# Performance work log

Measured on AMD Instinct MI355X. Metric: run time of the kernel, lower is better.

## Reference

```python
import jax, jax.numpy as jnp
import numpy as np

THETA = 10000.0


def apply_rope(t):
    """Partial rotary on first head_dim//2 dims, interleaved pairs (rotary_embedding_torch).
    t: (B, H, S, D) float32."""
    B, H, S, D = t.shape
    rot_dim = D // 2  # RotaryEmbedding(head_dim // 2)
    inv_freq = 1.0 / (THETA ** (jnp.arange(0, rot_dim, 2, dtype=jnp.float32) / rot_dim))  # (rot_dim//2,)
    pos = jnp.arange(S, dtype=jnp.float32)
    freqs = pos[:, None] * inv_freq[None, :]            # (S, rot_dim//2)
    freqs = jnp.repeat(freqs, 2, axis=-1)               # (S, rot_dim) interleaved
    cos, sin = jnp.cos(freqs), jnp.sin(freqs)           # (S, rot_dim)
    t_rot, t_pass = t[..., :rot_dim], t[..., rot_dim:]
    x1 = t_rot[..., 0::2]
    x2 = t_rot[..., 1::2]
    rot_half = jnp.stack((-x2, x1), axis=-1).reshape(t_rot.shape)
    t_rot = t_rot * cos + rot_half * sin
    return jnp.concatenate([t_rot, t_pass], axis=-1)


def setup_inputs() -> dict:
    key = jax.random.key(0)
    k1, k2, k3, k4, k5 = jax.random.split(key, 5)
    B, S, Dm = 2, 2048, 1024
    scale = 1.0 / np.sqrt(Dm)
    return {
        "x": jax.random.normal(k1, (B, S, Dm), dtype=jnp.float32),
        "Wqkv": jax.random.normal(k2, (3 * Dm, Dm), dtype=jnp.float32) * scale,
        "bqkv": jax.random.normal(k3, (3 * Dm,), dtype=jnp.float32) * 0.01,
        "Wout": jax.random.normal(k4, (Dm, Dm), dtype=jnp.float32) * scale,
        "bout": jax.random.normal(k5, (Dm,), dtype=jnp.float32) * 0.01,
    }


def reference(x, Wqkv, bqkv, Wout, bout):
    B, S, Dm = x.shape
    H = 16
    Dh = Dm // H
    qkv = x @ Wqkv.T + bqkv                              # (B, S, 3*Dm)
    qkv = qkv.reshape(B, S, 3, H, Dh).transpose(2, 0, 3, 1, 4)  # (3, B, H, S, Dh)
    q, k, v = qkv[0], qkv[1], qkv[2]
    q = apply_rope(q.astype(jnp.float32))
    k = apply_rope(k.astype(jnp.float32))
    scores = jnp.einsum("bhqd,bhkd->bhqk", q, k) / jnp.sqrt(jnp.float32(Dh))
    attn = jax.nn.softmax(scores, axis=-1)
    out = jnp.einsum("bhqk,bhkd->bhqd", attn, v)         # (B, H, S, Dh)
    out = out.transpose(0, 2, 1, 3).reshape(B, S, Dm)
    return out @ Wout.T + bout
```

## Files before the change

kernel.cpp:

```cpp
#include <hip/hip_runtime.h>

#define S_LEN 2048
#define DMODEL 1024
#define NHEAD 16
#define DHEAD 64
#define BATCH 2
#define BH_TOT (BATCH * NHEAD)
#define TOK (BATCH * S_LEN)
#define NQKV (3 * DMODEL)

#define QSCALE 0.18033688011112042f

typedef float  f32x4  __attribute__((ext_vector_type(4)));
typedef __bf16 bf16x8 __attribute__((ext_vector_type(8)));
typedef __bf16 bf16x4 __attribute__((ext_vector_type(4)));
typedef __bf16 bf16x2 __attribute__((ext_vector_type(2)));
typedef short  s16x4  __attribute__((ext_vector_type(4)));

typedef __attribute__((address_space(1))) void* as1_ptr;
typedef __attribute__((address_space(3))) void* as3_ptr;

__device__ __forceinline__ void gl2lds16(const void* g, void* l) {
  __builtin_amdgcn_global_load_lds((as1_ptr)(void*)g, (as3_ptr)l, 16, 0, 0);
}

__device__ __forceinline__ f32x4 mfma32(bf16x8 a, bf16x8 b, f32x4 c) {
  return __builtin_amdgcn_mfma_f32_16x16x32_bf16(a, b, c, 0, 0, 0);
}
__device__ __forceinline__ f32x4 mfma16(bf16x4 a, bf16x4 b, f32x4 c) {
  return __builtin_amdgcn_mfma_f32_16x16x16bf16_1k(
      __builtin_bit_cast(s16x4, a), __builtin_bit_cast(s16x4, b), c, 0, 0, 0);
}

__global__ __launch_bounds__(256) void cvt_kernel(const float* __restrict__ src,
                                                  __bf16* __restrict__ dst, int n) {
  const int i = (blockIdx.x * 256 + threadIdx.x) * 4;
  if (i >= n) return;
  const f32x4 v = *(const f32x4*)(src + i);
  bf16x4 o;
  o[0] = (__bf16)v[0]; o[1] = (__bf16)v[1]; o[2] = (__bf16)v[2]; o[3] = (__bf16)v[3];
  *(bf16x4*)(dst + i) = o;
}

__device__ __forceinline__ void gemm_tile_128(const __bf16* __restrict__ A,
                                              const __bf16* __restrict__ Bw,
                                              const int Kd, const int tileM, const int tileN,
                                              __bf16* As, __bf16* Bs, f32x4 acc[4][4]) {
  const int t    = threadIdx.x;
  const int lane = t & 63;
  const int wave = t >> 6;
  const int quad = lane >> 4;
  const int c    = lane & 15;
  const int wm   = (wave >> 1) << 6;
  const int wn   = (wave & 1) << 6;

  const int u0 = t, u1 = t + 256;
  const __bf16* gA0 = A  + (size_t)(tileM + (u0 >> 2)) * Kd + (u0 & 3) * 8;
  const __bf16* gA1 = A  + (size_t)(tileM + (u1 >> 2)) * Kd + (u1 & 3) * 8;
  const __bf16* gB0 = Bw + (size_t)(tileN + (u0 >> 2)) * Kd + (u0 & 3) * 8;
  const __bf16* gB1 = Bw + (size_t)(tileN + (u1 >> 2)) * Kd + (u1 & 3) * 8;
  __bf16* lA0 = As + u0 * 8; __bf16* lA1 = As + u1 * 8;
  __bf16* lB0 = Bs + u0 * 8; __bf16* lB1 = Bs + u1 * 8;

  for (int k0 = 0; k0 < Kd; k0 += 32) {
    gl2lds16(gA0 + k0, lA0);
    gl2lds16(gA1 + k0, lA1);
    gl2lds16(gB0 + k0, lB0);
    gl2lds16(gB1 + k0, lB1);
    __syncthreads();
    bf16x8 af[4], bfr[4];
#pragma unroll
    for (int mt = 0; mt < 4; ++mt)
      af[mt] = *(const bf16x8*)(As + (wm + mt * 16 + c) * 32 + quad * 8);
#pragma unroll
    for (int nt = 0; nt < 4; ++nt)
      bfr[nt] = *(const bf16x8*)(Bs + (wn + nt * 16 + c) * 32 + quad * 8);
#pragma unroll
    for (int mt = 0; mt < 4; ++mt)
#pragma unroll
      for (int nt = 0; nt < 4; ++nt)
        acc[mt][nt] = mfma32(af[mt], bfr[nt], acc[mt][nt]);
    __syncthreads();
  }
}

__global__ __launch_bounds__(256) void gemm_qkv_kernel(const __bf16* __restrict__ xb,
                                                       const __bf16* __restrict__ Wb,
                                                       const float* __restrict__ bias,
                                                       __bf16* __restrict__ Qb,
                                                       __bf16* __restrict__ Kb,
                                                       __bf16* __restrict__ Vtb) {
  __shared__ __align__(16) __bf16 As[128 * 32];
  __shared__ __align__(16) __bf16 Bs[128 * 32];
  f32x4 acc[4][4];
#pragma unroll
  for (int i = 0; i < 4; ++i)
#pragma unroll
    for (int j = 0; j < 4; ++j) acc[i][j] = (f32x4){0.f, 0.f, 0.f, 0.f};

  const int tileM = blockIdx.y * 128;
  const int tileN = blockIdx.x * 128;
  gemm_tile_128(xb, Wb, DMODEL, tileM, tileN, As, Bs, acc);

  const int t = threadIdx.x;
  const int lane = t & 63, wave = t >> 6;
  const int quad = lane >> 4, c = lane & 15;
  const int wm = (wave >> 1) << 6, wn = (wave & 1) << 6;

#pragma unroll
  for (int nt = 0; nt < 4; ++nt) {
    const int col = tileN + wn + nt * 16 + c;
    const float bv = bias[col];
    const int which = col >> 10;
    const int h  = (col >> 6) & 15;
    const int dh = col & 63;
    if (which == 2) {
#pragma unroll
      for (int mt = 0; mt < 4; ++mt) {
        const int row0 = tileM + wm + mt * 16 + quad * 4;
        const int bb = row0 >> 11;
        const int ss = row0 & (S_LEN - 1);
        bf16x4 o;
#pragma unroll
        for (int r = 0; r < 4; ++r) o[r] = (__bf16)(acc[mt][nt][r] + bv);
        *(bf16x4*)(Vtb + (((size_t)(bb * NHEAD + h)) * DHEAD + dh) * S_LEN + ss) = o;
      }
    } else {
      __bf16* dst = (which == 0) ? Qb : Kb;
      const float scl = (which == 0) ? QSCALE : 1.0f;
#pragma unroll
      for (int mt = 0; mt < 4; ++mt) {
#pragma unroll
        for (int r = 0; r < 4; ++r) {
          const int row = tileM + wm + mt * 16 + quad * 4 + r;
          const int bb = row >> 11;
          const int ss = row & (S_LEN - 1);
          dst[(((size_t)(bb * NHEAD + h)) * S_LEN + ss) * DHEAD + dh] =
              (__bf16)((acc[mt][nt][r] + bv) * scl);
        }
      }
    }
  }
}

__global__ __launch_bounds__(256) void gemm_out_kernel(const __bf16* __restrict__ AOb,
                                                       const __bf16* __restrict__ Wb,
                                                       const float* __restrict__ bout,
                                                       float* __restrict__ out) {
  __shared__ __align__(16) __bf16 As[128 * 32];
  __shared__ __align__(16) __bf16 Bs[128 * 32];
  f32x4 acc[4][4];
#pragma unroll
  for (int i = 0; i < 4; ++i)
#pragma unroll
    for (int j = 0; j < 4; ++j) acc[i][j] = (f32x4){0.f, 0.f, 0.f, 0.f};

  const int tileM = blockIdx.y * 128;
  const int tileN = blockIdx.x * 128;
  gemm_tile_128(AOb, Wb, DMODEL, tileM, tileN, As, Bs, acc);

  const int t = threadIdx.x;
  const int lane = t & 63, wave = t >> 6;
  const int quad = lane >> 4, c = lane & 15;
  const int wm = (wave >> 1) << 6, wn = (wave & 1) << 6;

#pragma unroll
  for (int nt = 0; nt < 4; ++nt) {
    const int col = tileN + wn + nt * 16 + c;
    const float bv = bout[col];
#pragma unroll
    for (int mt = 0; mt < 4; ++mt) {
#pragma unroll
      for (int r = 0; r < 4; ++r) {
        const int row = tileM + wm + mt * 16 + quad * 4 + r;
        out[(size_t)row * DMODEL + col] = acc[mt][nt][r] + bv;
      }
    }
  }
}

__global__ __launch_bounds__(256) void rope_kernel(__bf16* __restrict__ Qb, __bf16* __restrict__ Kb) {
  const int idx = blockIdx.x * 256 + threadIdx.x;
  const int j  = idx & 15;
  const int s  = (idx >> 4) & (S_LEN - 1);
  const int bh = (idx >> 15) & (BH_TOT - 1);
  __bf16* base = (idx >> 20) ? Kb : Qb;
  bf16x2* p = (bf16x2*)(base + ((size_t)bh * S_LEN + s) * DHEAD) + j;
  bf16x2 v = *p;
  const float x1 = (float)v[0];
  const float x2 = (float)v[1];
  const float LOG2_10000 = 13.287712379549449f;
  const float inv = exp2f(-(float)j * (LOG2_10000 / 16.0f));
  const float ang = (float)s * inv;
  float sn, cs;
  sincosf(ang, &sn, &cs);
  bf16x2 o;
  o[0] = (__bf16)(x1 * cs - x2 * sn);
  o[1] = (__bf16)(x2 * cs + x1 * sn);
  *p = o;
}

__global__ __launch_bounds__(256, 3) void attn_kernel(const __bf16* __restrict__ Qb,
                                                      const __bf16* __restrict__ Kb,
                                                      const __bf16* __restrict__ Vtb,
                                                      __bf16* __restrict__ AOb) {
  __shared__ __align__(16) float Os[64 * 68];
  __shared__ float Ls[4][4][16];

  const int qt = blockIdx.x;
  const int bh = blockIdx.y;
  const int b = bh >> 4, h = bh & 15;
  const int t = threadIdx.x, wave = t >> 6, lane = t & 63;
  const int quad = lane >> 4, c = lane & 15;
  const size_t head = (size_t)bh * S_LEN * DHEAD;
  const int q0 = qt * 64;

  bf16x8 qf[4][2];
#pragma unroll
  for (int nt = 0; nt < 4; ++nt) {
    const __bf16* qp = Qb + head + (size_t)(q0 + nt * 16 + c) * DHEAD + quad * 8;
    qf[nt][0] = *(const bf16x8*)qp;
    qf[nt][1] = *(const bf16x8*)(qp + 32);
  }

  f32x4 ot[4][4];
#pragma unroll
  for (int dt = 0; dt < 4; ++dt)
#pragma unroll
    for (int nt = 0; nt < 4; ++nt) ot[dt][nt] = (f32x4){0.f, 0.f, 0.f, 0.f};
  f32x4 lp = (f32x4){0.f, 0.f, 0.f, 0.f};

  const __bf16* kp = Kb + head + (size_t)(wave * 16 + c) * DHEAD + quad * 8;
  const __bf16* vp0 = Vtb + ((size_t)(bh * DHEAD) + c) * S_LEN + wave * 16 + quad * 4;

  bf16x8 kf0 = *(const bf16x8*)kp;
  bf16x8 kf1 = *(const bf16x8*)(kp + 32);
  bf16x4 vf[4];
#pragma unroll
  for (int dt = 0; dt < 4; ++dt)
    vf[dt] = *(const bf16x4*)(vp0 + (size_t)(dt * 16) * S_LEN);

  for (int kb = 0; kb < S_LEN / 64; ++kb) {
    bf16x8 nk0, nk1;
    bf16x4 nv[4];
    if (kb < S_LEN / 64 - 1) {
      const __bf16* kpn = kp + (size_t)(kb + 1) * 64 * DHEAD;
      nk0 = *(const bf16x8*)kpn;
      nk1 = *(const bf16x8*)(kpn + 32);
      const __bf16* vpn = vp0 + (kb + 1) * 64;
#pragma unroll
      for (int dt = 0; dt < 4; ++dt)
        nv[dt] = *(const bf16x4*)(vpn + (size_t)(dt * 16) * S_LEN);
    }

    bf16x4 pf[4];
#pragma unroll
    for (int nt = 0; nt < 4; ++nt) {
      f32x4 z = (f32x4){0.f, 0.f, 0.f, 0.f};
      z = mfma32(kf0, qf[nt][0], z);
      z = mfma32(kf1, qf[nt][1], z);
#pragma unroll
      for (int r = 0; r < 4; ++r) {
        const float p = __builtin_amdgcn_exp2f(z[r]);
        lp[nt] += p;
        pf[nt][r] = (__bf16)p;
      }
    }

#pragma unroll
    for (int dt = 0; dt < 4; ++dt)
#pragma unroll
      for (int nt = 0; nt < 4; ++nt)
        ot[dt][nt] = mfma16(vf[dt], pf[nt], ot[dt][nt]);

    kf0 = nk0; kf1 = nk1;
#pragma unroll
    for (int dt = 0; dt < 4; ++dt) vf[dt] = nv[dt];
  }

#pragma unroll
  for (int nt = 0; nt < 4; ++nt) {
    float v = lp[nt];
    v += __shfl_xor(v, 16);
    v += __shfl_xor(v, 32);
    if (lane < 16) Ls[wave][nt][lane] = v;
  }

  for (int w = 0; w < 4; ++w) {
    __syncthreads();
    if (wave == w) {
#pragma unroll
      for (int nt = 0; nt < 4; ++nt) {
#pragma unroll
        for (int dt = 0; dt < 4; ++dt) {
          float* p = Os + (nt * 16 + c) * 68 + dt * 16 + quad * 4;
          if (w == 0) *(f32x4*)p = ot[dt][nt];
          else        *(f32x4*)p = *(const f32x4*)p + ot[dt][nt];
        }
      }
    }
  }
  __syncthreads();

  const int q = t >> 2, dc = t & 3;
  const float lsum = Ls[0][q >> 4][q & 15] + Ls[1][q >> 4][q & 15] +
                     Ls[2][q >> 4][q & 15] + Ls[3][q >> 4][q & 15];
  const float inv = 1.0f / lsum;
  const float* orow = Os + q * 68 + dc * 16;
  f32x4 v0 = *(const f32x4*)(orow + 0);
  f32x4 v1 = *(const f32x4*)(orow + 4);
  f32x4 v2 = *(const f32x4*)(orow + 8);
  f32x4 v3 = *(const f32x4*)(orow + 12);
  bf16x8 o0, o1;
#pragma unroll
  for (int i = 0; i < 4; ++i) {
    o0[i]     = (__bf16)(v0[i] * inv);
    o0[i + 4] = (__bf16)(v1[i] * inv);
    o1[i]     = (__bf16)(v2[i] * inv);
    o1[i + 4] = (__bf16)(v3[i] * inv);
  }
  __bf16* dst = AOb + ((size_t)(b * S_LEN + q0 + q)) * DMODEL + h * DHEAD + dc * 16;
  *(bf16x8*)dst = o0;
  *(bf16x8*)(dst + 8) = o1;
}

extern "C" void kernel_launch(void* const* d_in, const int* in_sizes, int n_in,
                              void* d_out, int out_size, void* d_ws, size_t ws_size,
                              hipStream_t stream) {
  const float* x    = (const float*)d_in[0];
  const float* Wqkv = (const float*)d_in[1];
  const float* bqkv = (const float*)d_in[2];
  const float* Wout = (const float*)d_in[3];
  const float* bout = (const float*)d_in[4];
  float* out = (float*)d_out;

  char* ws = (char*)d_ws;
  __bf16* xb    = (__bf16*)(ws + 0);
  __bf16* Wqkvb = (__bf16*)(ws + (size_t)8  * 1024 * 1024);
  __bf16* Woutb = (__bf16*)(ws + (size_t)14 * 1024 * 1024);
  __bf16* Qb    = (__bf16*)(ws + (size_t)16 * 1024 * 1024);
  __bf16* Kb    = (__bf16*)(ws + (size_t)24 * 1024 * 1024);
  __bf16* Vtb   = (__bf16*)(ws + (size_t)32 * 1024 * 1024);
  __bf16* AOb   = (__bf16*)(ws + (size_t)40 * 1024 * 1024);

  cvt_kernel<<<(TOK * DMODEL) / 1024, 256, 0, stream>>>(x, xb, TOK * DMODEL);
  cvt_kernel<<<(NQKV * DMODEL) / 1024, 256, 0, stream>>>(Wqkv, Wqkvb, NQKV * DMODEL);
  cvt_kernel<<<(DMODEL * DMODEL) / 1024, 256, 0, stream>>>(Wout, Woutb, DMODEL * DMODEL);

  gemm_qkv_kernel<<<dim3(NQKV / 128, TOK / 128), 256, 0, stream>>>(xb, Wqkvb, bqkv, Qb, Kb, Vtb);

  rope_kernel<<<(2 * BH_TOT * S_LEN * 16) / 256, 256, 0, stream>>>(Qb, Kb);

  attn_kernel<<<dim3(S_LEN / 64, BH_TOT), 256, 0, stream>>>(Qb, Kb, Vtb, AOb);

  gemm_out_kernel<<<dim3(DMODEL / 128, TOK / 128), 256, 0, stream>>>(AOb, Woutb, bout, out);
}
```

Measured before the change: 248.3 us.

## Stage attention K/V tiles through swizzled double-buffered LDS and fuse conversion launches

The attention kernel now loads each 64-key K and V^T tile cooperatively with coalesced 16-byte global loads. It stores the tile into XOR-swizzled, double-buffered shared memory and reads the MFMA fragments from LDS, instead of each wave issuing its own narrow strided global loads. This adds a block barrier per key tile and raises shared memory to about 50 KB per block, which may limit occupancy. The three fp32-to-bf16 conversion launches are also merged into one kernel to cut launch overhead.

Result: faster. 211.3 us (-14.9%).

```diff
diff --git a/kernel.cpp b/kernel.cpp
--- a/kernel.cpp
+++ b/kernel.cpp
@@ -32,14 +32,26 @@
       __builtin_bit_cast(s16x4, a), __builtin_bit_cast(s16x4, b), c, 0, 0, 0);
 }
 
-__global__ __launch_bounds__(256) void cvt_kernel(const float* __restrict__ src,
-                                                  __bf16* __restrict__ dst, int n) {
+#define NX (TOK * DMODEL)
+#define NW1 (NQKV * DMODEL)
+#define NW2 (DMODEL * DMODEL)
+__global__ __launch_bounds__(256) void cvt_all_kernel(const float* __restrict__ x,
+                                                      const float* __restrict__ W1,
+                                                      const float* __restrict__ W2,
+                                                      __bf16* __restrict__ xb,
+                                                      __bf16* __restrict__ W1b,
+                                                      __bf16* __restrict__ W2b) {
   const int i = (blockIdx.x * 256 + threadIdx.x) * 4;
-  if (i >= n) return;
-  const f32x4 v = *(const f32x4*)(src + i);
+  const float* src;
+  __bf16* dst;
+  int off;
+  if (i < NX)            { src = x;  dst = xb;  off = i; }
+  else if (i < NX + NW1) { src = W1; dst = W1b; off = i - NX; }
+  else                   { src = W2; dst = W2b; off = i - NX - NW1; }
+  const f32x4 v = *(const f32x4*)(src + off);
   bf16x4 o;
   o[0] = (__bf16)v[0]; o[1] = (__bf16)v[1]; o[2] = (__bf16)v[2]; o[3] = (__bf16)v[3];
-  *(bf16x4*)(dst + i) = o;
+  *(bf16x4*)(dst + off) = o;
 }
 
 __device__ __forceinline__ void gemm_tile_128(const __bf16* __restrict__ A,
@@ -204,8 +216,11 @@
                                                       const __bf16* __restrict__ Kb,
                                                       const __bf16* __restrict__ Vtb,
                                                       __bf16* __restrict__ AOb) {
-  __shared__ __align__(16) float Os[64 * 68];
-  __shared__ float Ls[4][4][16];
+  extern __shared__ __align__(16) char smem[];
+  __bf16* KsB  = (__bf16*)smem;
+  __bf16* VtsB = (__bf16*)(smem + 16384);
+  float*  Os   = (float*)(smem + 32768);
+  float*  Ls   = (float*)(smem + 50176);
 
   const int qt = blockIdx.x;
   const int bh = blockIdx.y;
@@ -217,85 +232,110 @@
 
   bf16x8 qf[4][2];
 #pragma unroll
-  for (int nt = 0; nt < 4; ++nt) {
-    const __bf16* qp = Qb + head + (size_t)(q0 + nt * 16 + c) * DHEAD + quad * 8;
-    qf[nt][0] = *(const bf16x8*)qp;
-    qf[nt][1] = *(const bf16x8*)(qp + 32);
+  for (int nq = 0; nq < 4; ++nq) {
+    const __bf16* qp = Qb + head + (size_t)(q0 + nq * 16 + c) * DHEAD + quad * 8;
+    qf[nq][0] = *(const bf16x8*)qp;
+    qf[nq][1] = *(const bf16x8*)(qp + 32);
   }
 
   f32x4 ot[4][4];
 #pragma unroll
   for (int dt = 0; dt < 4; ++dt)
 #pragma unroll
-    for (int nt = 0; nt < 4; ++nt) ot[dt][nt] = (f32x4){0.f, 0.f, 0.f, 0.f};
-  f32x4 lp = (f32x4){0.f, 0.f, 0.f, 0.f};
-
-  const __bf16* kp = Kb + head + (size_t)(wave * 16 + c) * DHEAD + quad * 8;
-  const __bf16* vp0 = Vtb + ((size_t)(bh * DHEAD) + c) * S_LEN + wave * 16 + quad * 4;
-
-  bf16x8 kf0 = *(const bf16x8*)kp;
-  bf16x8 kf1 = *(const bf16x8*)(kp + 32);
-  bf16x4 vf[4];
-#pragma unroll
-  for (int dt = 0; dt < 4; ++dt)
-    vf[dt] = *(const bf16x4*)(vp0 + (size_t)(dt * 16) * S_LEN);
+    for (int nq = 0; nq < 4; ++nq) ot[dt][nq] = (f32x4){0.f, 0.f, 0.f, 0.f};
+  float lp[4] = {0.f, 0.f, 0.f, 0.f};
+
+  const int u0 = t, u1 = t + 256;
+  const int r0 = u0 >> 3, g0 = u0 & 7, sl0 = g0 ^ (r0 & 7);
+  const int r1 = u1 >> 3, g1 = u1 & 7, sl1 = g1 ^ (r1 & 7);
+  const __bf16* kg0 = Kb + head + (size_t)r0 * DHEAD + g0 * 8;
+  const __bf16* kg1 = Kb + head + (size_t)r1 * DHEAD + g1 * 8;
+  const __bf16* vg0 = Vtb + ((size_t)bh * DHEAD + r0) * S_LEN + g0 * 8;
+  const __bf16* vg1 = Vtb + ((size_t)bh * DHEAD + r1) * S_LEN + g1 * 8;
+  const int kd0 = r0 * 64 + sl0 * 8;
+  const int kd1 = r1 * 64 + sl1 * 8;
+
+  {
+    const bf16x8 a0 = *(const bf16x8*)kg0;
+    const bf16x8 a1 = *(const bf16x8*)kg1;
+    const bf16x8 b0 = *(const bf16x8*)vg0;
+    const bf16x8 b1 = *(const bf16x8*)vg1;
+    *(bf16x8*)(KsB + kd0) = a0;
+    *(bf16x8*)(KsB + kd1) = a1;
+    *(bf16x8*)(VtsB + kd0) = b0;
+    *(bf16x8*)(VtsB + kd1) = b1;
+  }
+
+  const int cxor = c & 7;
+  const int kArow = (wave * 16 + c) * 64;
+  const int vchunk = wave * 2 + (quad >> 1);
+  const int vsub = (quad & 1) * 4;
 
   for (int kb = 0; kb < S_LEN / 64; ++kb) {
-    bf16x8 nk0, nk1;
-    bf16x4 nv[4];
-    if (kb < S_LEN / 64 - 1) {
-      const __bf16* kpn = kp + (size_t)(kb + 1) * 64 * DHEAD;
-      nk0 = *(const bf16x8*)kpn;
-      nk1 = *(const bf16x8*)(kpn + 32);
-      const __bf16* vpn = vp0 + (kb + 1) * 64;
-#pragma unroll
-      for (int dt = 0; dt < 4; ++dt)
-        nv[dt] = *(const bf16x4*)(vpn + (size_t)(dt * 16) * S_LEN);
-    }
-
-    bf16x4 pf[4];
-#pragma unroll
-    for (int nt = 0; nt < 4; ++nt) {
+    __syncthreads();
+    const int cur = (kb & 1) * 4096;
+    const bool pre = (kb + 1 < S_LEN / 64);
+    bf16x8 pk0, pk1, pv0, pv1;
+    if (pre) {
+      const int k0n = (kb + 1) * 64;
+      pk0 = *(const bf16x8*)(kg0 + (size_t)k0n * DHEAD);
+      pk1 = *(const bf16x8*)(kg1 + (size_t)k0n * DHEAD);
+      pv0 = *(const bf16x8*)(vg0 + k0n);
+      pv1 = *(const bf16x8*)(vg1 + k0n);
+    }
+
+    const bf16x8 kA0 = *(const bf16x8*)(KsB + cur + kArow + ((0 + quad) ^ cxor) * 8);
+    const bf16x8 kA1 = *(const bf16x8*)(KsB + cur + kArow + ((4 + quad) ^ cxor) * 8);
+
+    bf16x4 vA[4];
+#pragma unroll
+    for (int dt = 0; dt < 4; ++dt)
+      vA[dt] = *(const bf16x4*)(VtsB + cur + (dt * 16 + c) * 64 + ((vchunk ^ cxor) * 8) + vsub);
+
+#pragma unroll
+    for (int nq = 0; nq < 4; ++nq) {
       f32x4 z = (f32x4){0.f, 0.f, 0.f, 0.f};
-      z = mfma32(kf0, qf[nt][0], z);
-      z = mfma32(kf1, qf[nt][1], z);
+      z = mfma32(kA0, qf[nq][0], z);
+      z = mfma32(kA1, qf[nq][1], z);
+      bf16x4 pf;
 #pragma unroll
       for (int r = 0; r < 4; ++r) {
         const float p = __builtin_amdgcn_exp2f(z[r]);
-        lp[nt] += p;
-        pf[nt][r] = (__bf16)p;
-      }
-    }
-
-#pragma unroll
-    for (int dt = 0; dt < 4; ++dt)
-#pragma unroll
-      for (int nt = 0; nt < 4; ++nt)
-        ot[dt][nt] = mfma16(vf[dt], pf[nt], ot[dt][nt]);
-
-    kf0 = nk0; kf1 = nk1;
-#pragma unroll
-    for (int dt = 0; dt < 4; ++dt) vf[dt] = nv[dt];
-  }
-
-#pragma unroll
-  for (int nt = 0; nt < 4; ++nt) {
-    float v = lp[nt];
+        lp[nq] += p;
+        pf[r] = (__bf16)p;
+      }
+#pragma unroll
+      for (int dt = 0; dt < 4; ++dt)
+        ot[dt][nq] = mfma16(vA[dt], pf, ot[dt][nq]);
+    }
+
+    if (pre) {
+      const int nxt = ((kb + 1) & 1) * 4096;
+      *(bf16x8*)(KsB + nxt + kd0) = pk0;
+      *(bf16x8*)(KsB + nxt + kd1) = pk1;
+      *(bf16x8*)(VtsB + nxt + kd0) = pv0;
+      *(bf16x8*)(VtsB + nxt + kd1) = pv1;
+    }
+  }
+
+#pragma unroll
+  for (int nq = 0; nq < 4; ++nq) {
+    float v = lp[nq];
     v += __shfl_xor(v, 16);
     v += __shfl_xor(v, 32);
-    if (lane < 16) Ls[wave][nt][lane] = v;
+    if (lane < 16) Ls[(wave * 4 + nq) * 16 + lane] = v;
   }
 
   for (int w = 0; w < 4; ++w) {
     __syncthreads();
     if (wave == w) {
 #pragma unroll
-      for (int nt = 0; nt < 4; ++nt) {
+      for (int nq = 0; nq < 4; ++nq) {
 #pragma unroll
         for (int dt = 0; dt < 4; ++dt) {
-          float* p = Os + (nt * 16 + c) * 68 + dt * 16 + quad * 4;
-          if (w == 0) *(f32x4*)p = ot[dt][nt];
-          else        *(f32x4*)p = *(const f32x4*)p + ot[dt][nt];
+          float* p = Os + (nq * 16 + c) * 68 + dt * 16 + quad * 4;
+          if (w == 0) *(f32x4*)p = ot[dt][nq];
+          else        *(f32x4*)p = *(const f32x4*)p + ot[dt][nq];
         }
       }
     }
@@ -303,8 +343,9 @@
   __syncthreads();
 
   const int q = t >> 2, dc = t & 3;
-  const float lsum = Ls[0][q >> 4][q & 15] + Ls[1][q >> 4][q & 15] +
-                     Ls[2][q >> 4][q & 15] + Ls[3][q >> 4][q & 15];
+  const int nq = q >> 4, cc = q & 15;
+  const float lsum = Ls[(0 * 4 + nq) * 16 + cc] + Ls[(1 * 4 + nq) * 16 + cc] +
+                     Ls[(2 * 4 + nq) * 16 + cc] + Ls[(3 * 4 + nq) * 16 + cc];
   const float inv = 1.0f / lsum;
   const float* orow = Os + q * 68 + dc * 16;
   f32x4 v0 = *(const f32x4*)(orow + 0);
@@ -343,15 +384,13 @@
   __bf16* Vtb   = (__bf16*)(ws + (size_t)32 * 1024 * 1024);
   __bf16* AOb   = (__bf16*)(ws + (size_t)40 * 1024 * 1024);
 
-  cvt_kernel<<<(TOK * DMODEL) / 1024, 256, 0, stream>>>(x, xb, TOK * DMODEL);
-  cvt_kernel<<<(NQKV * DMODEL) / 1024, 256, 0, stream>>>(Wqkv, Wqkvb, NQKV * DMODEL);
-  cvt_kernel<<<(DMODEL * DMODEL) / 1024, 256, 0, stream>>>(Wout, Woutb, DMODEL * DMODEL);
+  cvt_all_kernel<<<(NX + NW1 + NW2) / 1024, 256, 0, stream>>>(x, Wqkv, Wout, xb, Wqkvb, Woutb);
 
   gemm_qkv_kernel<<<dim3(NQKV / 128, TOK / 128), 256, 0, stream>>>(xb, Wqkvb, bqkv, Qb, Kb, Vtb);
 
   rope_kernel<<<(2 * BH_TOT * S_LEN * 16) / 256, 256, 0, stream>>>(Qb, Kb);
 
-  attn_kernel<<<dim3(S_LEN / 64, BH_TOT), 256, 0, stream>>>(Qb, Kb, Vtb, AOb);
+  attn_kernel<<<dim3(S_LEN / 64, BH_TOT), 256, 51200, stream>>>(Qb, Kb, Vtb, AOb);
 
   gemm_out_kernel<<<dim3(DMODEL / 128, TOK / 128), 256, 0, stream>>>(AOb, Woutb, bout, out);
 }
```
